# Kernel tuning notes

Measured on AMD Instinct MI355X. Metric: run time of the kernel, lower is better.

## Reference

```python
import jax, jax.numpy as jnp
import numpy as np

INPUT_DIM = 1024
TAGSET = 16
EMBED = 1024
HIDDEN = 2048
INTERM = 1024
T = 4096
START_IDX = 0  # y_codebook['__START__']


def setup_inputs() -> dict:
    key = jax.random.key(0)
    ks = jax.random.split(key, 11)
    def w(k, shape, fan_in):
        return (jax.random.normal(k, shape, jnp.float32) / np.sqrt(fan_in)).astype(jnp.float32)
    cat = INPUT_DIM + TAGSET  # x_t concatenated with one-hot of previous tag
    return {
        "seq": jax.random.normal(ks[0], (1, T, INPUT_DIM), jnp.float32),
        "W_embed": w(ks[1], (EMBED, cat), cat),
        "b_embed": jnp.zeros((EMBED,), jnp.float32),
        "W_ih": w(ks[2], (4 * HIDDEN, EMBED), EMBED),
        "W_hh": w(ks[3], (4 * HIDDEN, HIDDEN), HIDDEN),
        "b_ih": jnp.zeros((4 * HIDDEN,), jnp.float32),
        "b_hh": jnp.zeros((4 * HIDDEN,), jnp.float32),
        "W_interm": w(ks[4], (INTERM, HIDDEN), HIDDEN),
        "b_interm": jnp.zeros((INTERM,), jnp.float32),
        "W_tag": w(ks[5], (TAGSET, INTERM), INTERM),
        "b_tag": jnp.zeros((TAGSET,), jnp.float32),
    }


def _forward(seq, W_embed, b_embed, W_ih, W_hh, b_ih, b_hh, W_interm, b_interm, W_tag, b_tag):
    def step(carry, x_t):
        h, c, prev_oh = carry
        xin = jnp.concatenate([x_t, prev_oh])              # [INPUT_DIM+TAGSET]
        e = jax.nn.relu(W_embed @ xin + b_embed)           # embed + nonlinearity
        gates = W_ih @ e + b_ih + W_hh @ h + b_hh          # [4H], torch gate order i,f,g,o
        i, f, g, o = jnp.split(gates, 4)
        c = jax.nn.sigmoid(f) * c + jax.nn.sigmoid(i) * jnp.tanh(g)
        h = jax.nn.sigmoid(o) * jnp.tanh(c)
        inter = jax.nn.relu(W_interm @ h + b_interm)
        tag_space = W_tag @ inter + b_tag                  # [TAGSET]
        logp = jax.nn.log_softmax(tag_space)
        prob = jax.nn.softmax(tag_space)
        pred = jnp.argmax(logp)
        new_oh = jax.lax.stop_gradient(jax.nn.one_hot(pred, TAGSET, dtype=seq.dtype))
        return (h, c, new_oh), (logp, prob, pred)

    h0 = jnp.zeros((HIDDEN,), seq.dtype)
    c0 = jnp.zeros((HIDDEN,), seq.dtype)
    oh0 = jax.nn.one_hot(START_IDX, TAGSET, dtype=seq.dtype)
    _, (logps, probs, preds) = jax.lax.scan(step, (h0, c0, oh0), seq[0])
    return logps, probs, preds.astype(jnp.int32)


def reference(seq, W_embed, b_embed, W_ih, W_hh, b_ih, b_hh, W_interm, b_interm, W_tag, b_tag):
    return _forward(seq, W_embed, b_embed, W_ih, W_hh, b_ih, b_hh, W_interm, b_interm, W_tag, b_tag)
```

## Files before the change

### kernel.cpp

```cpp
#include <hip/hip_runtime.h>
#include <math.h>

#define T_STEPS 4096
#define EMB 1024
#define HID 2048
#define CAT 1040
#define TAG 16
#define NBLK 256
#define NTHR 1024
#define FLAG_STRIDE 32

#define OUT_LOGP 0
#define OUT_PROB (T_STEPS * TAG)
#define OUT_PRED (2 * T_STEPS * TAG)

__device__ __forceinline__ float sigf(float x) { return 1.0f / (1.0f + expf(-x)); }

__device__ __forceinline__ unsigned aloadu(const unsigned* p) {
  return __hip_atomic_load(p, __ATOMIC_RELAXED, __HIP_MEMORY_SCOPE_AGENT);
}
__device__ __forceinline__ void astoreu(unsigned* p, unsigned v) {
  __hip_atomic_store(p, v, __ATOMIC_RELAXED, __HIP_MEMORY_SCOPE_AGENT);
}
__device__ __forceinline__ float aloadf(const float* p) {
  return __hip_atomic_load(p, __ATOMIC_RELAXED, __HIP_MEMORY_SCOPE_AGENT);
}
__device__ __forceinline__ void astoref(float* p, float v) {
  __hip_atomic_store(p, v, __ATOMIC_RELAXED, __HIP_MEMORY_SCOPE_AGENT);
}
__device__ __forceinline__ unsigned long long aload64(const unsigned long long* p) {
  return __hip_atomic_load(p, __ATOMIC_RELAXED, __HIP_MEMORY_SCOPE_AGENT);
}
__device__ __forceinline__ void astore64(unsigned long long* p, unsigned long long v) {
  __hip_atomic_store(p, v, __ATOMIC_RELAXED, __HIP_MEMORY_SCOPE_AGENT);
}
__device__ __forceinline__ unsigned long long pack(unsigned ep, float v) {
  return ((unsigned long long)ep << 32) | (unsigned long long)__float_as_uint(v);
}
__device__ __forceinline__ float val32(unsigned long long v) {
  return __uint_as_float((unsigned)v);
}
__device__ __forceinline__ int epok(unsigned long long v, unsigned ep) {
  return (unsigned)(v >> 32) == ep;
}

__global__ __launch_bounds__(256) void rnnss_vt_kernel(const float* __restrict__ We,
                                                       float* __restrict__ VT) {
  int n = blockIdx.x * 256 + threadIdx.x;
  int p = n >> 10, i = n & 1023;
  VT[n] = We[(size_t)i * CAT + EMB + p];
}

__global__ __launch_bounds__(256) void rnnss_uprep(const float* __restrict__ X,
                                                   const float* __restrict__ W,
                                                   const float* __restrict__ be,
                                                   float* __restrict__ U) {
  __shared__ __align__(16) float As[32][68];
  __shared__ __align__(16) float Bs[32][68];
  const int bm = blockIdx.x * 64;
  const int bn = blockIdx.y * 64;
  const int tid = threadIdx.x;
  const int tx = tid & 15, ty = tid >> 4;
  const int lr = tid >> 5, lc = tid & 31;
  float acc[4][4] = {};
  for (int k0 = 0; k0 < EMB; k0 += 32) {
#pragma unroll
    for (int p = 0; p < 8; ++p) {
      As[lc][lr + 8 * p] = X[(size_t)(bm + lr + 8 * p) * EMB + k0 + lc];
      Bs[lc][lr + 8 * p] = W[(size_t)(bn + lr + 8 * p) * CAT + k0 + lc];
    }
    __syncthreads();
#pragma unroll 8
    for (int k = 0; k < 32; ++k) {
      const float4 a = *(const float4*)&As[k][ty * 4];
      const float4 v = *(const float4*)&Bs[k][tx * 4];
      float am[4] = {a.x, a.y, a.z, a.w};
      float bv[4] = {v.x, v.y, v.z, v.w};
#pragma unroll
      for (int m = 0; m < 4; ++m)
#pragma unroll
        for (int n = 0; n < 4; ++n) acc[m][n] = fmaf(am[m], bv[n], acc[m][n]);
    }
    __syncthreads();
  }
#pragma unroll
  for (int m = 0; m < 4; ++m)
#pragma unroll
    for (int n = 0; n < 4; ++n)
      U[(size_t)(bm + ty * 4 + m) * EMB + bn + tx * 4 + n] =
          acc[m][n] + be[bn + tx * 4 + n];
}

__global__ __launch_bounds__(NTHR, 4) void rnnss_persist(
    const float* __restrict__ Wih, const float* __restrict__ Whh,
    const float* __restrict__ bih, const float* __restrict__ bhh,
    const float* __restrict__ Witm, const float* __restrict__ bitm,
    const float* __restrict__ Wtag, const float* __restrict__ btag,
    const float* __restrict__ U, const float* __restrict__ VT,
    unsigned long long* __restrict__ hpay,
    float* __restrict__ tpg,
    unsigned* __restrict__ flags,
    float* __restrict__ out) {
  __shared__ __align__(16) float sWi[32 * 1024];
  __shared__ __align__(16) float se[EMB];
  __shared__ __align__(16) float sh[HID];
  __shared__ float sacc1[NTHR];
  __shared__ float sg[32];
  __shared__ float wpart[16];
  __shared__ float stv[TAG];
  __shared__ float sc[8];

  const int tid = threadIdx.x;
  const int b = blockIdx.x;
  const int u0 = b * 8;
  if (tid < 8) sc[tid] = 0.0f;
  sh[tid] = 0.0f;
  sh[tid + 1024] = 0.0f;
  sacc1[tid] = 0.0f;

  const int rt = tid >> 5;
  const int q = tid & 31;
  const int gsec = rt >> 3, j = rt & 7;
  const int grow = gsec * HID + u0 + j;
  const float bsum = bih[grow] + bhh[grow];
  const float4* __restrict__ wh = (const float4*)(Whh + (size_t)grow * HID);

  const int brow = tid >> 8, bq = tid & 255;
  const float4* __restrict__ wm = (const float4*)(Witm + (size_t)(b * 4 + brow) * HID);
  float bi0 = 0, bi1 = 0, bi2 = 0, bi3 = 0;
  float wt0 = 0, wt1 = 0, wt2 = 0, wt3 = 0;
  if (tid < TAG) {
    bi0 = bitm[b * 4 + 0];
    bi1 = bitm[b * 4 + 1];
    bi2 = bitm[b * 4 + 2];
    bi3 = bitm[b * 4 + 3];
    wt0 = Wtag[(size_t)tid * 1024 + b * 4 + 0];
    wt1 = Wtag[(size_t)tid * 1024 + b * 4 + 1];
    wt2 = Wtag[(size_t)tid * 1024 + b * 4 + 2];
    wt3 = Wtag[(size_t)tid * 1024 + b * 4 + 3];
  }
  float btw = 0.0f;
  if ((tid & 63) == 0) btw = btag[tid >> 6];

  {
    const float4* WiF = (const float4*)Wih;
    float4* sWiF = (float4*)sWi;
#pragma unroll
    for (int n = 0; n < 8; ++n) {
      int idx = tid + 1024 * n;
      int r = idx >> 8, c = idx & 255;
      int gr = (r >> 3) * HID + u0 + (r & 7);
      sWiF[idx] = WiF[(size_t)gr * 256 + c];
    }
  }

  float4 rwh[16], rwm[2];
#pragma unroll
  for (int it = 0; it < 16; ++it) rwh[it] = wh[q + 32 * it];
  rwm[0] = wm[bq];
  rwm[1] = wm[bq + 256];
#pragma unroll
  for (int it = 0; it < 16; ++it)
    asm volatile("" : "+v"(rwh[it].x), "+v"(rwh[it].y), "+v"(rwh[it].z), "+v"(rwh[it].w));
  asm volatile("" : "+v"(rwm[0].x), "+v"(rwm[0].y), "+v"(rwm[0].z), "+v"(rwm[0].w));
  asm volatile("" : "+v"(rwm[1].x), "+v"(rwm[1].y), "+v"(rwm[1].z), "+v"(rwm[1].w));

  const float4* sef = (const float4*)se;
  const float4* shf = (const float4*)sh;
  const float4* sWiF4 = (const float4*)sWi;

  int pred = 0;
  float u_cur = U[tid];
  __syncthreads();

  for (int t = 0; t < T_STEPS; ++t) {
    const unsigned ep = (unsigned)t + 1u;

    {
      float ev = u_cur + VT[(size_t)pred * EMB + tid];
      se[tid] = ev > 0.0f ? ev : 0.0f;
    }
    __syncthreads();
    float acc0 = 0.0f;
#pragma unroll
    for (int it = 0; it < 8; ++it) {
      float4 w = sWiF4[rt * 256 + q + 32 * it], x = sef[q + 32 * it];
      acc0 += w.x * x.x + w.y * x.y + w.z * x.z + w.w * x.w;
    }
    float acc = acc0 + sacc1[tid];
#pragma unroll
    for (int d = 16; d > 0; d >>= 1) acc += __shfl_down(acc, d, 32);
    if (q == 0) sg[rt] = acc + bsum;
    __syncthreads();
    if (tid < 8) {
      float iv = sigf(sg[tid]);
      float fv = sigf(sg[8 + tid]);
      float gv = tanhf(sg[16 + tid]);
      float ov = sigf(sg[24 + tid]);
      float c = fv * sc[tid] + iv * gv;
      sc[tid] = c;
      astore64(hpay + u0 + tid, pack(ep, ov * tanhf(c)));
    }

    {
      const int lane = tid & 63;
      const int base = (tid >> 6) * 128 + lane;
      const unsigned long long* hp = hpay + base;
      unsigned long long v0 = aload64(hp);
      unsigned long long v1 = aload64(hp + 64);
      while (!epok(v0, ep)) { __builtin_amdgcn_s_sleep(1); v0 = aload64(hp); }
      while (!epok(v1, ep)) { __builtin_amdgcn_s_sleep(1); v1 = aload64(hp + 64); }
      sh[base] = val32(v0);
      sh[base + 64] = val32(v1);
    }
    float u_nxt = (t + 1 < T_STEPS) ? U[(size_t)(t + 1) * EMB + tid] : 0.0f;
    __syncthreads();

    {
      float a2 = 0.0f;
      float4 w = rwm[0], x = shf[bq];
      a2 += w.x * x.x + w.y * x.y + w.z * x.z + w.w * x.w;
      w = rwm[1]; x = shf[bq + 256];
      a2 += w.x * x.x + w.y * x.y + w.z * x.z + w.w * x.w;
#pragma unroll
      for (int d = 32; d > 0; d >>= 1) a2 += __shfl_down(a2, d, 64);
      if ((tid & 63) == 0) wpart[tid >> 6] = a2;
    }
    __syncthreads();
    if (tid < TAG) {
      float i0 = wpart[0] + wpart[1] + wpart[2] + wpart[3] + bi0;
      float i1 = wpart[4] + wpart[5] + wpart[6] + wpart[7] + bi1;
      float i2 = wpart[8] + wpart[9] + wpart[10] + wpart[11] + bi2;
      float i3 = wpart[12] + wpart[13] + wpart[14] + wpart[15] + bi3;
      i0 = i0 > 0.0f ? i0 : 0.0f;
      i1 = i1 > 0.0f ? i1 : 0.0f;
      i2 = i2 > 0.0f ? i2 : 0.0f;
      i3 = i3 > 0.0f ? i3 : 0.0f;
      astoref(tpg + tid * NBLK + b, wt0 * i0 + wt1 * i1 + wt2 * i2 + wt3 * i3);
    }
    if (tid == 0) {
      asm volatile("s_waitcnt vmcnt(0)" ::: "memory");
      astoreu(flags + (size_t)b * FLAG_STRIDE, ep);
    }

    {
      float a1 = 0.0f;
#pragma unroll
      for (int it = 0; it < 16; ++it) {
        float4 w = rwh[it], x = shf[q + 32 * it];
        a1 += w.x * x.x + w.y * x.y + w.z * x.z + w.w * x.w;
      }
      sacc1[tid] = a1;
    }

    if (tid < NBLK) {
      const unsigned* f = flags + (size_t)tid * FLAG_STRIDE;
      while (aloadu(f) < ep) __builtin_amdgcn_s_sleep(1);
    }
    asm volatile("" ::: "memory");
    __syncthreads();

    {
      const int w = tid >> 6, l = tid & 63;
      float v = aloadf(tpg + w * NBLK + l) + aloadf(tpg + w * NBLK + 64 + l) +
                aloadf(tpg + w * NBLK + 128 + l) + aloadf(tpg + w * NBLK + 192 + l);
#pragma unroll
      for (int d = 32; d > 0; d >>= 1) v += __shfl_down(v, d, 64);
      if (l == 0) stv[w] = v + btw;
    }
    __syncthreads();
    {
      int am = 0;
      float bv = stv[0];
#pragma unroll
      for (int k = 1; k < TAG; ++k) {
        if (stv[k] > bv) { bv = stv[k]; am = k; }
      }
      pred = am;
      if (b == 0) {
        if (tid < TAG) {
          float m = stv[0];
#pragma unroll
          for (int k = 1; k < TAG; ++k) m = fmaxf(m, stv[k]);
          float s = expf(stv[tid] - m);
#pragma unroll
          for (int msk = 8; msk > 0; msk >>= 1) s += __shfl_xor(s, msk, 16);
          float ls = logf(s);
          float lp = stv[tid] - m - ls;
          out[OUT_LOGP + t * TAG + tid] = lp;
          out[OUT_PROB + t * TAG + tid] = expf(lp);
        } else if (tid == TAG) {
          out[OUT_PRED + t] = (float)am;
        }
      }
      u_cur = u_nxt;
    }
  }
}

extern "C" void kernel_launch(void* const* d_in, const int* in_sizes, int n_in,
                              void* d_out, int out_size, void* d_ws, size_t ws_size,
                              hipStream_t stream) {
  const float* seq = (const float*)d_in[0];
  const float* W_embed = (const float*)d_in[1];
  const float* b_embed = (const float*)d_in[2];
  const float* W_ih = (const float*)d_in[3];
  const float* W_hh = (const float*)d_in[4];
  const float* b_ih = (const float*)d_in[5];
  const float* b_hh = (const float*)d_in[6];
  const float* W_interm = (const float*)d_in[7];
  const float* b_interm = (const float*)d_in[8];
  const float* W_tag = (const float*)d_in[9];
  const float* b_tag = (const float*)d_in[10];
  (void)in_sizes; (void)n_in; (void)out_size; (void)ws_size;

  const size_t flg_b = (size_t)NBLK * FLAG_STRIDE * 4;
  const size_t hp_b = (size_t)HID * 8;
  const size_t tp_b = (size_t)TAG * NBLK * 4;
  const size_t vt_b = (size_t)TAG * EMB * 4;

  char* ws = (char*)d_ws;
  unsigned* flags = (unsigned*)ws;
  unsigned long long* hpay = (unsigned long long*)(ws + flg_b);
  float* tpg = (float*)(ws + flg_b + hp_b);
  float* VT = (float*)(ws + flg_b + hp_b + tp_b);
  float* U = (float*)(ws + flg_b + hp_b + tp_b + vt_b);
  float* out = (float*)d_out;

  hipMemsetAsync(ws, 0, flg_b + hp_b, stream);

  hipLaunchKernelGGL(rnnss_vt_kernel, dim3((TAG * EMB) / 256), dim3(256), 0, stream,
                     W_embed, VT);
  hipLaunchKernelGGL(rnnss_uprep, dim3(T_STEPS / 64, EMB / 64), dim3(256), 0, stream,
                     seq, W_embed, b_embed, U);

  void* args[] = {
      (void*)&W_ih,    (void*)&W_hh,  (void*)&b_ih,  (void*)&b_hh,
      (void*)&W_interm,(void*)&b_interm, (void*)&W_tag, (void*)&b_tag,
      (void*)&U,       (void*)&VT,    (void*)&hpay,  (void*)&tpg,
      (void*)&flags,   (void*)&out};
  hipLaunchCooperativeKernel((const void*)rnnss_persist, dim3(NBLK), dim3(NTHR),
                             args, 0, stream);
}
```

Measured before the change: 33.19 ms.

## Replace per-block flag barrier with epoch-tagged tag partial payloads

Each block's tag-score partial is now published as a 64-bit value packed with its epoch. Readers spin on each payload directly, which removes the separate flag array, the vmcnt wait, the flag-polling loop and one __syncthreads per step. The prefetch of the next step's U row is also moved ahead of the hidden-state spin wait so its latency overlaps the wait. The cost is twice the bytes in the tag partial buffer and more scattered polling loads per thread.

```diff
diff --git a/kernel.cpp b/kernel.cpp
--- a/kernel.cpp
+++ b/kernel.cpp
@@ -8,7 +8,6 @@
 #define TAG 16
 #define NBLK 256
 #define NTHR 1024
-#define FLAG_STRIDE 32
 
 #define OUT_LOGP 0
 #define OUT_PROB (T_STEPS * TAG)
@@ -16,18 +15,6 @@
 
 __device__ __forceinline__ float sigf(float x) { return 1.0f / (1.0f + expf(-x)); }
 
-__device__ __forceinline__ unsigned aloadu(const unsigned* p) {
-  return __hip_atomic_load(p, __ATOMIC_RELAXED, __HIP_MEMORY_SCOPE_AGENT);
-}
-__device__ __forceinline__ void astoreu(unsigned* p, unsigned v) {
-  __hip_atomic_store(p, v, __ATOMIC_RELAXED, __HIP_MEMORY_SCOPE_AGENT);
-}
-__device__ __forceinline__ float aloadf(const float* p) {
-  return __hip_atomic_load(p, __ATOMIC_RELAXED, __HIP_MEMORY_SCOPE_AGENT);
-}
-__device__ __forceinline__ void astoref(float* p, float v) {
-  __hip_atomic_store(p, v, __ATOMIC_RELAXED, __HIP_MEMORY_SCOPE_AGENT);
-}
 __device__ __forceinline__ unsigned long long aload64(const unsigned long long* p) {
   return __hip_atomic_load(p, __ATOMIC_RELAXED, __HIP_MEMORY_SCOPE_AGENT);
 }
@@ -98,8 +85,7 @@
     const float* __restrict__ Wtag, const float* __restrict__ btag,
     const float* __restrict__ U, const float* __restrict__ VT,
     unsigned long long* __restrict__ hpay,
-    float* __restrict__ tpg,
-    unsigned* __restrict__ flags,
+    unsigned long long* __restrict__ tp64,
     float* __restrict__ out) {
   __shared__ __align__(16) float sWi[32 * 1024];
   __shared__ __align__(16) float se[EMB];
@@ -202,6 +188,8 @@
       astore64(hpay + u0 + tid, pack(ep, ov * tanhf(c)));
     }
 
+    float u_nxt = (t + 1 < T_STEPS) ? U[(size_t)(t + 1) * EMB + tid] : 0.0f;
+
     {
       const int lane = tid & 63;
       const int base = (tid >> 6) * 128 + lane;
@@ -213,7 +201,6 @@
       sh[base] = val32(v0);
       sh[base + 64] = val32(v1);
     }
-    float u_nxt = (t + 1 < T_STEPS) ? U[(size_t)(t + 1) * EMB + tid] : 0.0f;
     __syncthreads();
 
     {
@@ -236,11 +223,8 @@
       i1 = i1 > 0.0f ? i1 : 0.0f;
       i2 = i2 > 0.0f ? i2 : 0.0f;
       i3 = i3 > 0.0f ? i3 : 0.0f;
-      astoref(tpg + tid * NBLK + b, wt0 * i0 + wt1 * i1 + wt2 * i2 + wt3 * i3);
-    }
-    if (tid == 0) {
-      asm volatile("s_waitcnt vmcnt(0)" ::: "memory");
-      astoreu(flags + (size_t)b * FLAG_STRIDE, ep);
+      astore64(tp64 + tid * NBLK + b,
+               pack(ep, wt0 * i0 + wt1 * i1 + wt2 * i2 + wt3 * i3));
     }
 
     {
@@ -253,22 +237,24 @@
       sacc1[tid] = a1;
     }
 
-    if (tid < NBLK) {
-      const unsigned* f = flags + (size_t)tid * FLAG_STRIDE;
-      while (aloadu(f) < ep) __builtin_amdgcn_s_sleep(1);
-    }
-    asm volatile("" ::: "memory");
-    __syncthreads();
-
     {
       const int w = tid >> 6, l = tid & 63;
-      float v = aloadf(tpg + w * NBLK + l) + aloadf(tpg + w * NBLK + 64 + l) +
-                aloadf(tpg + w * NBLK + 128 + l) + aloadf(tpg + w * NBLK + 192 + l);
+      const unsigned long long* tp = tp64 + w * NBLK;
+      unsigned long long p0 = aload64(tp + l);
+      unsigned long long p1 = aload64(tp + 64 + l);
+      unsigned long long p2 = aload64(tp + 128 + l);
+      unsigned long long p3 = aload64(tp + 192 + l);
+      while (!epok(p0, ep)) { __builtin_amdgcn_s_sleep(1); p0 = aload64(tp + l); }
+      while (!epok(p1, ep)) { __builtin_amdgcn_s_sleep(1); p1 = aload64(tp + 64 + l); }
+      while (!epok(p2, ep)) { __builtin_amdgcn_s_sleep(1); p2 = aload64(tp + 128 + l); }
+      while (!epok(p3, ep)) { __builtin_amdgcn_s_sleep(1); p3 = aload64(tp + 192 + l); }
+      float v = val32(p0) + val32(p1) + val32(p2) + val32(p3);
 #pragma unroll
       for (int d = 32; d > 0; d >>= 1) v += __shfl_down(v, d, 64);
       if (l == 0) stv[w] = v + btw;
     }
     __syncthreads();
+
     {
       int am = 0;
       float bv = stv[0];
@@ -314,20 +300,18 @@
   const float* b_tag = (const float*)d_in[10];
   (void)in_sizes; (void)n_in; (void)out_size; (void)ws_size;
 
-  const size_t flg_b = (size_t)NBLK * FLAG_STRIDE * 4;
   const size_t hp_b = (size_t)HID * 8;
-  const size_t tp_b = (size_t)TAG * NBLK * 4;
+  const size_t tp_b = (size_t)TAG * NBLK * 8;
   const size_t vt_b = (size_t)TAG * EMB * 4;
 
   char* ws = (char*)d_ws;
-  unsigned* flags = (unsigned*)ws;
-  unsigned long long* hpay = (unsigned long long*)(ws + flg_b);
-  float* tpg = (float*)(ws + flg_b + hp_b);
-  float* VT = (float*)(ws + flg_b + hp_b + tp_b);
-  float* U = (float*)(ws + flg_b + hp_b + tp_b + vt_b);
+  unsigned long long* hpay = (unsigned long long*)ws;
+  unsigned long long* tp64 = (unsigned long long*)(ws + hp_b);
+  float* VT = (float*)(ws + hp_b + tp_b);
+  float* U = (float*)(ws + hp_b + tp_b + vt_b);
   float* out = (float*)d_out;
 
-  hipMemsetAsync(ws, 0, flg_b + hp_b, stream);
+  hipMemsetAsync(ws, 0, hp_b + tp_b, stream);
 
   hipLaunchKernelGGL(rnnss_vt_kernel, dim3((TAG * EMB) / 256), dim3(256), 0, stream,
                      W_embed, VT);
@@ -337,8 +321,8 @@
   void* args[] = {
       (void*)&W_ih,    (void*)&W_hh,  (void*)&b_ih,  (void*)&b_hh,
       (void*)&W_interm,(void*)&b_interm, (void*)&W_tag, (void*)&b_tag,
-      (void*)&U,       (void*)&VT,    (void*)&hpay,  (void*)&tpg,
-      (void*)&flags,   (void*)&out};
+      (void*)&U,       (void*)&VT,    (void*)&hpay,  (void*)&tp64,
+      (void*)&out};
   hipLaunchCooperativeKernel((const void*)rnnss_persist, dim3(NBLK), dim3(NTHR),
                              args, 0, stream);
 }
```

Measured after the change: 28.59 ms, median of 2. 1.16x faster.
